# Kernel tuning notes

Measured on AMD Instinct MI355X. Metric: run time of the kernel, lower is better.

The kernel has to match this reference:

```python
import jax, jax.numpy as jnp
import numpy as np

B, C_IN, C_OUT = 2, 64, 64
NLAT_IN, NLON_IN = 181, 360
NLAT_OUT, NLON_OUT = 181, 360
KERNEL_SIZE = 9            # piecewise-linear basis, kernel_shape=(3,4): (3-1)*4+1
NNZ_PER = 24               # sparse neighbor entries per (kernel fn, output latitude)
NNZ = KERNEL_SIZE * NLAT_OUT * NNZ_PER


def setup_inputs() -> dict:
    key = jax.random.key(0)
    ks = jax.random.split(key, 6)
    x = jax.random.normal(ks[0], (B, C_IN, NLAT_IN, NLON_IN), jnp.float32)
    # quadrature-merged, normalized filter values (positive, O(1/support) scale)
    psi_vals = jax.random.uniform(ks[1], (NNZ,), jnp.float32) / NNZ_PER
    # structured sparse pattern: every (kernel, lat_out) pair has NNZ_PER neighbors
    psi_ker = jnp.repeat(jnp.arange(KERNEL_SIZE, dtype=jnp.int32), NLAT_OUT * NNZ_PER)
    psi_lat_out = jnp.tile(jnp.repeat(jnp.arange(NLAT_OUT, dtype=jnp.int32), NNZ_PER), KERNEL_SIZE)
    dlat = jax.random.randint(ks[2], (NNZ,), -1, 2, dtype=jnp.int32)
    psi_lat_in = jnp.clip(psi_lat_out + dlat, 0, NLAT_IN - 1)
    psi_lon_in = jax.random.randint(ks[3], (NNZ,), 0, NLON_IN, dtype=jnp.int32)
    scale = (1.0 / (C_IN * KERNEL_SIZE)) ** 0.5
    weight = scale * jax.random.normal(ks[4], (C_OUT, C_IN, KERNEL_SIZE), jnp.float32)
    bias = jnp.zeros((C_OUT,), jnp.float32)
    return dict(x=x, psi_vals=psi_vals, weight=weight, bias=bias,
                psi_ker=psi_ker, psi_lat_out=psi_lat_out,
                psi_lat_in=psi_lat_in, psi_lon_in=psi_lon_in)


def _disco_contraction(x, psi_vals, psi_ker, psi_lat_out, psi_lat_in, psi_lon_in):
    """Sparse DISCO contraction: y[b,c,k,lat_out,p] = sum_e psi_vals[e] *
    x[b,c,lat_in_e,(lon_in_e + p*pscale) % nlon_in]  for entries with (k_e, lat_out_e).
    Mirrors torch-harmonics' roll-and-sparse-bmm loop over output longitudes."""
    b, c, nlat_in, nlon_in = x.shape
    pscale = nlon_in // NLON_OUT
    xf = x.reshape(b * c, nlat_in, nlon_in)          # [BC, nlat_in, nlon_in]
    seg = psi_ker * NLAT_OUT + psi_lat_out           # [NNZ] segment id = (k, lat_out)
    nseg = KERNEL_SIZE * NLAT_OUT

    def one_shift(p):
        lon = (psi_lon_in + p * pscale) % nlon_in    # rolled longitude per entry
        g = xf[:, psi_lat_in, lon] * psi_vals        # [BC, NNZ] gather-multiply
        return jax.ops.segment_sum(g.T, seg, num_segments=nseg)  # [nseg, BC]

    ys = jax.lax.map(one_shift, jnp.arange(NLON_OUT))            # [NLON_OUT, nseg, BC]
    y = ys.transpose(1, 0, 2).reshape(KERNEL_SIZE, NLAT_OUT, NLON_OUT, b, c)
    return y.transpose(3, 4, 0, 1, 2)                # [B, C_in, K, nlat_out, nlon_out]


def reference(x, psi_vals, weight, bias, psi_ker, psi_lat_out, psi_lat_in, psi_lon_in):
    y = _disco_contraction(x, psi_vals, psi_ker, psi_lat_out, psi_lat_in, psi_lon_in)
    # groups=1: weight is [C_out, C_in, K]
    out = jnp.einsum("bckxy,fck->bfxy", y, weight)
    out = out + bias[None, :, None, None]
    return out
```

## Files before the change

### kernel.cpp

```cpp
#include <hip/hip_runtime.h>


#define NB    2
#define CIN   64
#define COUT  64
#define KS    9
#define NLAT  181
#define NLON  360
#define NPER  24

typedef _Float16 f16;
typedef _Float16 f16x8 __attribute__((ext_vector_type(8)));
typedef float    f32x4 __attribute__((ext_vector_type(4)));
typedef unsigned int u32;
typedef unsigned short u16;
typedef u32 u32x4 __attribute__((ext_vector_type(4)));

#define ROWB      23040
#define XT_BYTES  ((size_t)NB * 2 * NLAT * NLON * 32 * 2)
#define WT_BYTES  (KS * 64 * 64 * 2)
#define NMETA     (KS * NLAT * NPER)
#define XS_BYTES  (3 * ROWB)

#define U0  (NB * 2 * 4 * NLAT * NLON)
#define G0  ((U0 + 255) / 256)
#define G1  ((KS * 4096 + 255) / 256)
#define G2  ((NMETA + 255) / 256)

__global__ __launch_bounds__(256) void prep_kernel(
    const float* __restrict__ x, const float* __restrict__ weight,
    const float* __restrict__ psi_vals, const int* __restrict__ psi_lat_in,
    const int* __restrict__ psi_lon_in,
    f16* __restrict__ xT, f16* __restrict__ wT, int4* __restrict__ meta)
{
    const int bid = blockIdx.x, tid = threadIdx.x;
    if (bid < G0) {
        const int u = bid * 256 + tid;
        if (u >= U0) return;
        const int oct = u & 3;
        const int v   = u >> 2;
        const int lon = v % NLON;
        const int w   = v / NLON;
        const int lat = w % NLAT;
        const int z   = w / NLAT;
        const int h   = z & 1, b = z >> 1;
        const float* src = x + ((size_t)(b * CIN + h * 32 + oct * 8) * NLAT + lat) * NLON + lon;
        f16x8 vv;
#pragma unroll
        for (int j = 0; j < 8; ++j)
            vv[j] = (f16)src[(size_t)j * NLAT * NLON];
        const int op = oct ^ ((lon >> 1) & 3);
        *(f16x8*)&xT[(((size_t)z * NLAT + lat) * NLON + lon) * 32 + op * 8] = vv;
        return;
    }
    if (bid < G0 + G1) {
        const int e = (bid - G0) * 256 + tid;
        if (e < KS * 4096) {
            int c = e & 63, f = (e >> 6) & 63, k = e >> 12;
            wT[e] = (f16)weight[((size_t)(f * 64 + c)) * KS + k];
        }
        return;
    }
    {
        const int e = (bid - G0 - G1) * 256 + tid;
        if (e < NMETA) {
            int lat = (e / NPER) % NLAT;
            f16 pvh = (f16)psi_vals[e];
            u32 pb = (u32)__builtin_bit_cast(u16, pvh);
            int lonb = psi_lon_in[e] << 6;
            int4 m;
            m.x = (int)((pb << 16) | pb);
            m.y = (psi_lat_in[e] - lat + 1) * ROWB + lonb;
            m.z = lonb;
            m.w = 0;
            meta[e] = m;
        }
    }
}

__global__ __launch_bounds__(768, 6) void disco_main(
    const f16* __restrict__ xT, const f16* __restrict__ wT,
    const int4* __restrict__ meta, const float* __restrict__ bias,
    float* __restrict__ out)
{
    extern __shared__ char xs[];
    const int tid  = threadIdx.x;
    const int lane = tid & 63, wave = tid >> 6;
    const int pn   = lane & 15, q = lane >> 4;
    const int half2 = blockIdx.x, lat = blockIdx.y, b = blockIdx.z;

    const int tile = half2 * 12 + wave;
    const bool act = tile < 23;
    const int p  = tile * 16 + pn;
    const int pl = p >= NLON ? p - NLON : p;
    const u32 plq  = (u32)((pl << 6) + (q << 4));
    const u32 plqm = plq - (u32)ROWB;
    const u32 thr  = (u32)((NLON - pl) << 6);

    int rr0 = lat > 0 ? lat - 1 : 0;
    int rr2 = lat < NLAT - 1 ? lat + 1 : NLAT - 1;

    f32x4 D[4];
#pragma unroll
    for (int ft = 0; ft < 4; ++ft) D[ft] = (f32x4){0.f, 0.f, 0.f, 0.f};

    for (int h = 0; h < 2; ++h) {
        __syncthreads();
        {
            const size_t hb = (size_t)(b * 2 + h) * NLAT;
            const f16* s0 = xT + (hb + rr0) * NLON * 32;
            const f16* s1 = xT + (hb + lat) * NLON * 32;
            const f16* s2 = xT + (hb + rr2) * NLON * 32;
            for (int i = tid; i < 1440; i += 768) {
                *(f16x8*)&xs[i * 16]             = *(const f16x8*)&s0[i * 8];
                *(f16x8*)&xs[ROWB + i * 16]      = *(const f16x8*)&s1[i * 8];
                *(f16x8*)&xs[2 * ROWB + i * 16]  = *(const f16x8*)&s2[i * 8];
            }
        }
        __syncthreads();

        if (act) {
            for (int k = 0; k < KS; ++k) {
                f16x8 acc = (f16x8){0, 0, 0, 0, 0, 0, 0, 0};
                const int4* mp = meta + (k * NLAT + lat) * NPER;
#pragma unroll
                for (int tg = 0; tg < NPER; tg += 8) {
                    int4 m[8];
#pragma unroll
                    for (int j = 0; j < 8; ++j) m[j] = mp[tg + j];

                    u32 addr[8];
#pragma unroll
                    for (int j = 0; j < 8; ++j) {
                        u32 ad = ((u32)m[j].z >= thr) ? plqm : plq;
                        u32 a  = (u32)m[j].y + ad;
                        addr[j] = a ^ ((a >> 3) & 48u);
                    }
                    f16x8 xv[8];
#pragma unroll
                    for (int j = 0; j < 8; ++j)
                        xv[j] = *(const f16x8*)(xs + addr[j]);
#pragma unroll
                    for (int j = 0; j < 8; ++j) {
                        u32 pk = (u32)m[j].x;
                        u32x4 pkv = {pk, pk, pk, pk};
                        acc += xv[j] * __builtin_bit_cast(f16x8, pkv);
                    }
                }

                f16x8 Af[4];
                const f16* wk = wT + (size_t)k * 4096 + h * 32 + q * 8;
#pragma unroll
                for (int ft = 0; ft < 4; ++ft)
                    Af[ft] = *(const f16x8*)&wk[(ft * 16 + pn) * 64];
#pragma unroll
                for (int ft = 0; ft < 4; ++ft)
                    D[ft] = __builtin_amdgcn_mfma_f32_16x16x32_f16(Af[ft], acc, D[ft], 0, 0, 0);
            }
        }
    }

    if (act && p < NLON) {
#pragma unroll
        for (int ft = 0; ft < 4; ++ft)
#pragma unroll
            for (int r = 0; r < 4; ++r) {
                const int f = ft * 16 + q * 4 + r;
                out[((size_t)(b * COUT + f) * NLAT + lat) * NLON + p] = D[ft][r] + bias[f];
            }
    }
}

extern "C" void kernel_launch(void* const* d_in, const int* in_sizes, int n_in,
                              void* d_out, int out_size, void* d_ws, size_t ws_size,
                              hipStream_t stream) {
    const float* x          = (const float*)d_in[0];
    const float* psi_vals   = (const float*)d_in[1];
    const float* weight     = (const float*)d_in[2];
    const float* bias       = (const float*)d_in[3];
    const int*   psi_lat_in = (const int*)d_in[6];
    const int*   psi_lon_in = (const int*)d_in[7];
    float* out = (float*)d_out;

    f16*  xT   = (f16*)d_ws;
    f16*  wT   = (f16*)((char*)d_ws + XT_BYTES);
    int4* meta = (int4*)((char*)d_ws + XT_BYTES + WT_BYTES);

    (void)hipFuncSetAttribute((const void*)disco_main,
                              hipFuncAttributeMaxDynamicSharedMemorySize, XS_BYTES);

    prep_kernel<<<dim3(G0 + G1 + G2), 256, 0, stream>>>(
        x, weight, psi_vals, psi_lat_in, psi_lon_in, xT, wT, meta);
    disco_main<<<dim3(2, NLAT, NB), 768, XS_BYTES, stream>>>(
        xT, wT, meta, bias, out);
}
```

Before: 190.5 us.

## Stage all 64 channels per row in LDS and drop the two-pass channel-half loop

The transposed input now packs all 64 input channels per (lat, lon) into one 128-byte record with a new XOR swizzle, so each block loads three full rows (about 135 KB of LDS) once instead of twice for two channel halves. The gather loop reads two 16-byte chunks per neighbor entry and reuses the metadata load and address math for both halves, feeding two MFMAs per kernel function. The prep kernel also reads input pairs with 8-byte vector loads. The larger LDS footprint cuts blocks per CU (launch bounds drop from 6 to 3), so latency hiding may suffer.

```diff
diff --git a/kernel.cpp b/kernel.cpp
--- a/kernel.cpp
+++ b/kernel.cpp
@@ -12,17 +12,18 @@
 typedef _Float16 f16;
 typedef _Float16 f16x8 __attribute__((ext_vector_type(8)));
 typedef float    f32x4 __attribute__((ext_vector_type(4)));
+typedef float    f32x2 __attribute__((ext_vector_type(2)));
 typedef unsigned int u32;
 typedef unsigned short u16;
 typedef u32 u32x4 __attribute__((ext_vector_type(4)));
 
-#define ROWB      23040
-#define XT_BYTES  ((size_t)NB * 2 * NLAT * NLON * 32 * 2)
+#define ROWB      46080
+#define XT_BYTES  ((size_t)NB * NLAT * NLON * 64 * 2)
 #define WT_BYTES  (KS * 64 * 64 * 2)
 #define NMETA     (KS * NLAT * NPER)
 #define XS_BYTES  (3 * ROWB)
 
-#define U0  (NB * 2 * 4 * NLAT * NLON)
+#define U0  (NB * NLAT * 180 * 8)
 #define G0  ((U0 + 255) / 256)
 #define G1  ((KS * 4096 + 255) / 256)
 #define G2  ((NMETA + 255) / 256)
@@ -37,20 +38,25 @@
     if (bid < G0) {
         const int u = bid * 256 + tid;
         if (u >= U0) return;
-        const int oct = u & 3;
-        const int v   = u >> 2;
-        const int lon = v % NLON;
-        const int w   = v / NLON;
-        const int lat = w % NLAT;
-        const int z   = w / NLAT;
-        const int h   = z & 1, b = z >> 1;
-        const float* src = x + ((size_t)(b * CIN + h * 32 + oct * 8) * NLAT + lat) * NLON + lon;
-        f16x8 vv;
-#pragma unroll
-        for (int j = 0; j < 8; ++j)
-            vv[j] = (f16)src[(size_t)j * NLAT * NLON];
-        const int op = oct ^ ((lon >> 1) & 3);
-        *(f16x8*)&xT[(((size_t)z * NLAT + lat) * NLON + lon) * 32 + op * 8] = vv;
+        const int ch   = u & 7;
+        const int v    = u >> 3;
+        const int lon2 = v % 180;
+        const int w    = v / 180;
+        const int lat  = w % NLAT;
+        const int b    = w / NLAT;
+        const int lon0 = lon2 * 2;
+        const float* src = x + ((size_t)(b * CIN + ch * 8) * NLAT + lat) * NLON + lon0;
+        f16x8 v0, v1;
+#pragma unroll
+        for (int j = 0; j < 8; ++j) {
+            const f32x2 lv = *(const f32x2*)&src[(size_t)j * NLAT * NLON];
+            v0[j] = (f16)lv[0];
+            v1[j] = (f16)lv[1];
+        }
+        const int pos0 = ch ^ (lon0 & 7);
+        f16* xd = xT + ((size_t)(b * NLAT + lat) * NLON + lon0) * 64;
+        *(f16x8*)&xd[pos0 * 8]            = v0;
+        *(f16x8*)&xd[64 + (pos0 ^ 1) * 8] = v1;
         return;
     }
     if (bid < G0 + G1) {
@@ -67,7 +73,7 @@
             int lat = (e / NPER) % NLAT;
             f16 pvh = (f16)psi_vals[e];
             u32 pb = (u32)__builtin_bit_cast(u16, pvh);
-            int lonb = psi_lon_in[e] << 6;
+            int lonb = psi_lon_in[e] << 7;
             int4 m;
             m.x = (int)((pb << 16) | pb);
             m.y = (psi_lat_in[e] - lat + 1) * ROWB + lonb;
@@ -78,7 +84,7 @@
     }
 }
 
-__global__ __launch_bounds__(768, 6) void disco_main(
+__global__ __launch_bounds__(768, 3) void disco_main(
     const f16* __restrict__ xT, const f16* __restrict__ wT,
     const int4* __restrict__ meta, const float* __restrict__ bias,
     float* __restrict__ out)
@@ -93,69 +99,76 @@
     const bool act = tile < 23;
     const int p  = tile * 16 + pn;
     const int pl = p >= NLON ? p - NLON : p;
-    const u32 plq  = (u32)((pl << 6) + (q << 4));
+    const u32 plq  = (u32)((pl << 7) + (q << 4));
     const u32 plqm = plq - (u32)ROWB;
-    const u32 thr  = (u32)((NLON - pl) << 6);
-
-    int rr0 = lat > 0 ? lat - 1 : 0;
-    int rr2 = lat < NLAT - 1 ? lat + 1 : NLAT - 1;
+    const u32 thr  = (u32)((NLON - pl) << 7);
+
+    const int rr0 = lat > 0 ? lat - 1 : 0;
+    const int rr2 = lat < NLAT - 1 ? lat + 1 : NLAT - 1;
+
+    {
+        const size_t bb = (size_t)b * NLAT;
+        const f16* s0 = xT + (bb + rr0) * NLON * 64;
+        const f16* s1 = xT + (bb + lat) * NLON * 64;
+        const f16* s2 = xT + (bb + rr2) * NLON * 64;
+        for (int i = tid; i < 2880; i += 768) {
+            *(f16x8*)&xs[i * 16]             = *(const f16x8*)&s0[i * 8];
+            *(f16x8*)&xs[ROWB + i * 16]      = *(const f16x8*)&s1[i * 8];
+            *(f16x8*)&xs[2 * ROWB + i * 16]  = *(const f16x8*)&s2[i * 8];
+        }
+    }
+    __syncthreads();
 
     f32x4 D[4];
 #pragma unroll
     for (int ft = 0; ft < 4; ++ft) D[ft] = (f32x4){0.f, 0.f, 0.f, 0.f};
 
-    for (int h = 0; h < 2; ++h) {
-        __syncthreads();
-        {
-            const size_t hb = (size_t)(b * 2 + h) * NLAT;
-            const f16* s0 = xT + (hb + rr0) * NLON * 32;
-            const f16* s1 = xT + (hb + lat) * NLON * 32;
-            const f16* s2 = xT + (hb + rr2) * NLON * 32;
-            for (int i = tid; i < 1440; i += 768) {
-                *(f16x8*)&xs[i * 16]             = *(const f16x8*)&s0[i * 8];
-                *(f16x8*)&xs[ROWB + i * 16]      = *(const f16x8*)&s1[i * 8];
-                *(f16x8*)&xs[2 * ROWB + i * 16]  = *(const f16x8*)&s2[i * 8];
-            }
-        }
-        __syncthreads();
-
-        if (act) {
-            for (int k = 0; k < KS; ++k) {
-                f16x8 acc = (f16x8){0, 0, 0, 0, 0, 0, 0, 0};
-                const int4* mp = meta + (k * NLAT + lat) * NPER;
-#pragma unroll
-                for (int tg = 0; tg < NPER; tg += 8) {
-                    int4 m[8];
-#pragma unroll
-                    for (int j = 0; j < 8; ++j) m[j] = mp[tg + j];
-
-                    u32 addr[8];
-#pragma unroll
-                    for (int j = 0; j < 8; ++j) {
-                        u32 ad = ((u32)m[j].z >= thr) ? plqm : plq;
-                        u32 a  = (u32)m[j].y + ad;
-                        addr[j] = a ^ ((a >> 3) & 48u);
-                    }
-                    f16x8 xv[8];
-#pragma unroll
-                    for (int j = 0; j < 8; ++j)
-                        xv[j] = *(const f16x8*)(xs + addr[j]);
-#pragma unroll
-                    for (int j = 0; j < 8; ++j) {
-                        u32 pk = (u32)m[j].x;
-                        u32x4 pkv = {pk, pk, pk, pk};
-                        acc += xv[j] * __builtin_bit_cast(f16x8, pkv);
-                    }
+    if (act) {
+        for (int k = 0; k < KS; ++k) {
+            f16x8 acc0 = (f16x8){0, 0, 0, 0, 0, 0, 0, 0};
+            f16x8 acc1 = (f16x8){0, 0, 0, 0, 0, 0, 0, 0};
+            const int4* mp = meta + (k * NLAT + lat) * NPER;
+#pragma unroll
+            for (int tg = 0; tg < NPER; tg += 4) {
+                int4 m[4];
+#pragma unroll
+                for (int j = 0; j < 4; ++j) m[j] = mp[tg + j];
+
+                u32 a0[4], a1[4];
+#pragma unroll
+                for (int j = 0; j < 4; ++j) {
+                    u32 ad = ((u32)m[j].z >= thr) ? plqm : plq;
+                    u32 t  = (u32)m[j].y + ad;
+                    u32 a  = t ^ ((t >> 3) & 0x70u);
+                    a0[j] = a;
+                    a1[j] = a ^ 64u;
                 }
-
-                f16x8 Af[4];
-                const f16* wk = wT + (size_t)k * 4096 + h * 32 + q * 8;
-#pragma unroll
-                for (int ft = 0; ft < 4; ++ft)
-                    Af[ft] = *(const f16x8*)&wk[(ft * 16 + pn) * 64];
-#pragma unroll
-                for (int ft = 0; ft < 4; ++ft)
-                    D[ft] = __builtin_amdgcn_mfma_f32_16x16x32_f16(Af[ft], acc, D[ft], 0, 0, 0);
+                f16x8 xv0[4], xv1[4];
+#pragma unroll
+                for (int j = 0; j < 4; ++j) xv0[j] = *(const f16x8*)(xs + a0[j]);
+#pragma unroll
+                for (int j = 0; j < 4; ++j) xv1[j] = *(const f16x8*)(xs + a1[j]);
+#pragma unroll
+                for (int j = 0; j < 4; ++j) {
+                    u32 pk = (u32)m[j].x;
+                    u32x4 pkv = {pk, pk, pk, pk};
+                    f16x8 pf = __builtin_bit_cast(f16x8, pkv);
+                    acc0 += xv0[j] * pf;
+                    acc1 += xv1[j] * pf;
+                }
+            }
+
+            f16x8 Af0[4], Af1[4];
+            const f16* wk = wT + (size_t)k * 4096 + q * 8;
+#pragma unroll
+            for (int ft = 0; ft < 4; ++ft) {
+                Af0[ft] = *(const f16x8*)&wk[(ft * 16 + pn) * 64];
+                Af1[ft] = *(const f16x8*)&wk[32 + (ft * 16 + pn) * 64];
+            }
+#pragma unroll
+            for (int ft = 0; ft < 4; ++ft) {
+                D[ft] = __builtin_amdgcn_mfma_f32_16x16x32_f16(Af0[ft], acc0, D[ft], 0, 0, 0);
+                D[ft] = __builtin_amdgcn_mfma_f32_16x16x32_f16(Af1[ft], acc1, D[ft], 0, 0, 0);
             }
         }
     }
```

New measurement: 195.3 us. 1.02x slower.
